# Kernel optimization log

Measured on AMD Instinct MI355X. Metric: run time of the kernel, lower is better.

The kernel has to match this reference:

```python
import jax, jax.numpy as jnp
import numpy as np

B, S, D = 2, 2048, 1024
H, KH = 16, 4            # query heads, kv heads
DK = D // H              # 64
REP = H // KH            # queries per kv head


def _rope(x):
    # x: (B, h, S, dk); non-interleaved rotate-half RoPE as in source
    dk = x.shape[-1]
    half = dk // 2
    seq = x.shape[2]
    theta = 10000.0 ** (-(jnp.arange(half, dtype=jnp.float32) / half))
    pos = jnp.arange(seq, dtype=jnp.float32)
    freqs = pos[:, None] * theta[None, :]          # (S, half)
    cos = jnp.cos(freqs)[None, None]               # (1,1,S,half)
    sin = jnp.sin(freqs)[None, None]
    x1, x2 = x[..., :half], x[..., half:]
    return jnp.concatenate([x1 * cos - x2 * sin, x2 * cos + x1 * sin], axis=-1)


def setup_inputs() -> dict:
    key = jax.random.key(0)
    ks = jax.random.split(key, 9)
    sd = 1.0 / np.sqrt(D)
    x = jax.random.normal(ks[0], (B, S, D), dtype=jnp.float32)
    # causal mask: 1 where attend allowed, 0 where masked (mask==0 -> -inf)
    mask = jnp.tril(jnp.ones((S, S), dtype=jnp.int32))[None, None]
    Wq = jax.random.normal(ks[1], (D, H * DK), dtype=jnp.float32) * sd
    bq = jnp.zeros((H * DK,), dtype=jnp.float32)
    Wk = jax.random.normal(ks[2], (D, KH * DK), dtype=jnp.float32) * sd
    bk = jnp.zeros((KH * DK,), dtype=jnp.float32)
    Wv = jax.random.normal(ks[3], (D, KH * DK), dtype=jnp.float32) * sd
    bv = jnp.zeros((KH * DK,), dtype=jnp.float32)
    Wo = jax.random.normal(ks[4], (H * DK, D), dtype=jnp.float32) * sd
    bo = jnp.zeros((D,), dtype=jnp.float32)
    return {"x": x, "mask": mask, "Wq": Wq, "bq": bq, "Wk": Wk, "bk": bk,
            "Wv": Wv, "bv": bv, "Wo": Wo, "bo": bo}


def reference(x, mask, Wq, bq, Wk, bk, Wv, bv, Wo, bo):
    b, s, _ = x.shape
    q = (x @ Wq + bq).reshape(b, s, H, DK).transpose(0, 2, 1, 3)   # (B,H,S,DK)
    k = (x @ Wk + bk).reshape(b, s, KH, DK).transpose(0, 2, 1, 3)  # (B,KH,S,DK)
    v = (x @ Wv + bv).reshape(b, s, KH, DK).transpose(0, 2, 1, 3)
    q = _rope(q)
    k = _rope(k)
    k = jnp.repeat(k, REP, axis=1)  # GQA expand: (B,H,S,DK)
    v = jnp.repeat(v, REP, axis=1)
    attn = jnp.einsum('bhqd,bhkd->bhqk', q, k) / np.sqrt(DK).astype(np.float32)
    attn = jnp.where(mask == 0, -jnp.inf, attn)
    score = jax.nn.softmax(attn, axis=-1)
    out = jnp.einsum('bhqk,bhkd->bhqd', score, v)   # (B,H,S,DK)
    out = out.transpose(0, 2, 1, 3).reshape(b, s, H * DK)
    return out @ Wo + bo
```

## Files before the change

### kernel.cpp

```cpp
#include <hip/hip_runtime.h>
#include <math.h>

#define B_   2
#define S_   2048
#define D_   1024
#define H_   16
#define KH_  4
#define DK_  64

using bf16x8 = __attribute__((ext_vector_type(8))) short;
using bf16x4 = __attribute__((ext_vector_type(4))) short;
using f32x4  = __attribute__((ext_vector_type(4))) float;
using u32x4  = __attribute__((ext_vector_type(4))) unsigned int;
using u32x2  = __attribute__((ext_vector_type(2))) unsigned int;

__device__ inline unsigned short f2bf(float f) {
    unsigned u = __float_as_uint(f);
    u += 0x7FFFu + ((u >> 16) & 1u);
    return (unsigned short)(u >> 16);
}
__device__ inline float bf2f(unsigned short u) {
    return __uint_as_float(((unsigned)u) << 16);
}

#ifdef __has_builtin
#if __has_builtin(__builtin_amdgcn_cvt_pk_bf16_f32)
#define PKBF16 1
#endif
#if __has_builtin(__builtin_amdgcn_exp2f)
#define NEXP2 1
#endif
#endif
__device__ inline unsigned pk2bf(float a, float b) {
#ifdef PKBF16
    auto r = __builtin_amdgcn_cvt_pk_bf16_f32(a, b);
    unsigned u; __builtin_memcpy(&u, &r, 4);
    return u;
#else
    return (unsigned)f2bf(a) | ((unsigned)f2bf(b) << 16);
#endif
}
__device__ inline float fexp2(float x) {
#ifdef NEXP2
    return __builtin_amdgcn_exp2f(x);
#else
    return exp2f(x);
#endif
}

#define GL16(gp, lp) __builtin_amdgcn_global_load_lds( \
    (const __attribute__((address_space(1))) unsigned int*)(gp), \
    (__attribute__((address_space(3))) unsigned int*)(lp), 16, 0, 0)

__global__ __launch_bounds__(256) void prep_kernel(
    const float* __restrict__ x,
    const float* __restrict__ Wq, const float* __restrict__ Wk,
    const float* __restrict__ Wv, const float* __restrict__ Wo,
    unsigned short* __restrict__ xb,
    unsigned short* __restrict__ WqkvT,
    unsigned short* __restrict__ WoT)
{
    __shared__ float T[64][65];
    const int t = threadIdx.x;
    int bx = blockIdx.x;

    if (bx < 2048) {
        const int i = bx * 256 + t;
        f32x4 a = *(const f32x4*)(x + (long)i * 8);
        f32x4 b = *(const f32x4*)(x + (long)i * 8 + 4);
        bf16x8 o;
        o[0] = (short)f2bf(a[0]); o[1] = (short)f2bf(a[1]);
        o[2] = (short)f2bf(a[2]); o[3] = (short)f2bf(a[3]);
        o[4] = (short)f2bf(b[0]); o[5] = (short)f2bf(b[1]);
        o[6] = (short)f2bf(b[2]); o[7] = (short)f2bf(b[3]);
        *(bf16x8*)(xb + (long)i * 8) = o;
        return;
    }
    bx -= 2048;
    const float* in; unsigned short* out; int C;
    if (bx < 256)      { in = Wq; out = WqkvT;               C = 1024; }
    else if (bx < 320) { in = Wk; out = WqkvT + 1024 * 1024; C = 256;  bx -= 256; }
    else if (bx < 384) { in = Wv; out = WqkvT + 1280 * 1024; C = 256;  bx -= 320; }
    else               { in = Wo; out = WoT;                 C = 1024; bx -= 384; }
    const int R  = 1024, nr = 16;
    const int r0 = (bx % nr) * 64;
    const int c0 = (bx / nr) * 64;
    {
        const int r  = t >> 2;
        const int cq = (t & 3) * 16;
        const float* src = in + (long)(r0 + r) * C + c0 + cq;
        #pragma unroll
        for (int i = 0; i < 4; ++i) {
            f32x4 v = *(const f32x4*)(src + i * 4);
            T[r][cq + i * 4 + 0] = v[0];
            T[r][cq + i * 4 + 1] = v[1];
            T[r][cq + i * 4 + 2] = v[2];
            T[r][cq + i * 4 + 3] = v[3];
        }
    }
    __syncthreads();
    {
        const int c  = t >> 2;
        const int rq = (t & 3) * 16;
        bf16x8 p0, p1;
        #pragma unroll
        for (int i = 0; i < 8; ++i) {
            p0[i] = (short)f2bf(T[rq + i][c]);
            p1[i] = (short)f2bf(T[rq + 8 + i][c]);
        }
        unsigned short* dst = out + (long)(c0 + c) * R + r0 + rq;
        *(bf16x8*)dst       = p0;
        *(bf16x8*)(dst + 8) = p1;
    }
}

template<bool BF16OUT>
__global__ __launch_bounds__(256) void gemm64_kernel(
    const unsigned short* __restrict__ A,
    const unsigned short* __restrict__ Bt,
    const float* __restrict__ b0,
    const float* __restrict__ b1,
    const float* __restrict__ b2,
    float* __restrict__ outf,
    unsigned short* __restrict__ outb,
    int N, int K)
{
    __shared__ unsigned short As[2][64][64];
    __shared__ unsigned short Bs[2][128][64];

    const int t  = threadIdx.x;
    const int m0 = blockIdx.x * 64;
    const int n0 = blockIdx.y * 128;

    const int w    = t >> 6;
    const int lane = t & 63;
    const int n    = lane & 15;
    const int quad = lane >> 4;
    const int wm   = (w >> 1) * 32;
    const int wn   = (w & 1) * 64;

    const int sr8 = lane >> 3;
    const int gch = (lane & 7) ^ sr8;

    const unsigned short* gA = A  + (long)(m0 + w * 8 + sr8) * K + gch * 8;
    const unsigned short* gB = Bt + (long)(n0 + w * 8 + sr8) * K + gch * 8;

    #define STAGE(buf, kk)                                              \
    do {                                                                \
        GL16(gA + (kk),              &As[buf][w * 8][0]);               \
        GL16(gA + 32 * K + (kk),     &As[buf][w * 8 + 32][0]);          \
        GL16(gB + (kk),              &Bs[buf][w * 8][0]);               \
        GL16(gB + 32 * K + (kk),     &Bs[buf][w * 8 + 32][0]);          \
        GL16(gB + 64 * K + (kk),     &Bs[buf][w * 8 + 64][0]);          \
        GL16(gB + 96 * K + (kk),     &Bs[buf][w * 8 + 96][0]);          \
    } while (0)

    STAGE(0, 0);

    f32x4 acc[2][4];
    #pragma unroll
    for (int i = 0; i < 2; ++i)
        #pragma unroll
        for (int j = 0; j < 4; ++j) acc[i][j] = 0.0f;

    const int n7 = n & 7;

    for (int k0 = 0; k0 < K; k0 += 64) {
        const int cur = (k0 >> 6) & 1;
        __syncthreads();
        if (k0 + 64 < K) STAGE(cur ^ 1, k0 + 64);

        #pragma unroll
        for (int kp = 0; kp < 2; ++kp) {
            const int ca = ((kp * 4 + quad) ^ n7) * 8;
            bf16x8 af[2], bfr[4];
            #pragma unroll
            for (int i = 0; i < 2; ++i)
                af[i] = *(const bf16x8*)&As[cur][wm + i * 16 + n][ca];
            #pragma unroll
            for (int j = 0; j < 4; ++j)
                bfr[j] = *(const bf16x8*)&Bs[cur][wn + j * 16 + n][ca];
            #pragma unroll
            for (int mi = 0; mi < 2; ++mi)
                #pragma unroll
                for (int ni = 0; ni < 4; ++ni)
                    acc[mi][ni] = __builtin_amdgcn_mfma_f32_16x16x32_bf16(
                        af[mi], bfr[ni], acc[mi][ni], 0, 0, 0);
        }
    }
    #undef STAGE

    #pragma unroll
    for (int mi = 0; mi < 2; ++mi) {
        #pragma unroll
        for (int r = 0; r < 4; ++r) {
            const int gm = m0 + wm + mi * 16 + quad * 4 + r;
            #pragma unroll
            for (int ni = 0; ni < 4; ++ni) {
                const int gn = n0 + wn + ni * 16 + n;
                if (BF16OUT) {
                    const float b = (gn < 1024) ? b0[gn]
                                  : (gn < 1280) ? b1[gn - 1024]
                                                : b2[gn - 1280];
                    outb[(long)gm * N + gn] = f2bf(acc[mi][ni][r] + b);
                } else {
                    outf[(long)gm * N + gn] = acc[mi][ni][r] + b0[gn];
                }
            }
        }
    }
}

__global__ __launch_bounds__(256) void scatter_kernel(
    const unsigned short* __restrict__ qkvm,
    unsigned short* __restrict__ qbuf,
    unsigned short* __restrict__ kbuf,
    unsigned short* __restrict__ vbuf)
{
    __shared__ unsigned short T[64][72];
    const int t = threadIdx.x;
    int bx = blockIdx.x;

    if (bx < 1280) {
        const int idx = bx * 256 + t;
        const int m   = idx / 80;
        const int rem = idx - m * 80;
        const int h20 = rem >> 2;
        const int d0  = (rem & 3) * 8;

        const int s  = m & (S_ - 1);
        const int bb = m >> 11;
        const int col0 = (h20 < 16) ? h20 * 64 + d0 : 1024 + (h20 - 16) * 64 + d0;
        const float scl = (h20 < 16) ? 0.1803368801111606f : 1.0f;

        const bf16x8 x1v = *(const bf16x8*)(qkvm + (long)m * 1536 + col0);
        const bf16x8 x2v = *(const bf16x8*)(qkvm + (long)m * 1536 + col0 + 32);
        bf16x8 o1, o2;
        #pragma unroll
        for (int j = 0; j < 8; ++j) {
            const int d = d0 + j;
            const float theta = exp2f(-(float)d * (13.287712379549449f / 32.0f));
            const float f = (float)s * theta;
            const float c = cosf(f) * scl, sn = sinf(f) * scl;
            const float x1 = bf2f((unsigned short)x1v[j]);
            const float x2 = bf2f((unsigned short)x2v[j]);
            o1[j] = (short)f2bf(x1 * c - x2 * sn);
            o2[j] = (short)f2bf(x2 * c + x1 * sn);
        }
        unsigned short* dst = (h20 < 16)
            ? qbuf + ((long)(bb * H_ + h20) * S_ + s) * DK_ + d0
            : kbuf + ((long)(bb * KH_ + (h20 - 16)) * S_ + s) * DK_ + d0;
        *(bf16x8*)dst        = o1;
        *(bf16x8*)(dst + 32) = o2;
        return;
    }
    bx -= 1280;
    const int bkh = bx >> 5;
    const int s0  = (bx & 31) * 64;
    {
        const int s  = t >> 2;
        const int dq = (t & 3) * 16;
        const unsigned short* src =
            qkvm + (long)((bkh >> 2) * S_ + s0 + s) * 1536 + 1280 + (bkh & 3) * 64 + dq;
        *(bf16x8*)&T[s][dq]     = *(const bf16x8*)src;
        *(bf16x8*)&T[s][dq + 8] = *(const bf16x8*)(src + 8);
    }
    __syncthreads();
    {
        const int d  = t >> 2;
        const int sq = (t & 3) * 16;
        bf16x8 p0, p1;
        #pragma unroll
        for (int i = 0; i < 8; ++i) {
            p0[i] = (short)T[sq + i][d];
            p1[i] = (short)T[sq + 8 + i][d];
        }
        unsigned short* dst = vbuf + ((long)bkh * DK_ + d) * S_ + s0 + sq;
        *(bf16x8*)dst       = p0;
        *(bf16x8*)(dst + 8) = p1;
    }
}

__global__ __launch_bounds__(512) void attn_kernel(
    const unsigned short* __restrict__ qb,
    const unsigned short* __restrict__ kbf,
    const unsigned short* __restrict__ vT,
    unsigned short* __restrict__ ot)
{
    __shared__ __align__(16) unsigned short Ks[2][64][64];
    __shared__ __align__(16) unsigned short Vs[2][64][64];
    __shared__ __align__(16) unsigned short Ps[8][16][64];

    const int tid = threadIdx.x;
    const int bx  = blockIdx.x;

    const int j  = bx >> 8;
    const int p  = bx & 255;
    const int g  = p >> 5;
    const int bh = p & 31;
    const int a  = j ? g : (15 - g);

    const int b   = bh >> 4, h = bh & 15;
    const int kh  = h >> 2;
    const int q0  = a * 128;

    const int wv   = tid >> 6;
    const int lane = tid & 63;
    const int n    = lane & 15;
    const int quad = lane >> 4;
    const int xk   = n & 7;

    const unsigned short* qp =
        qb + ((long)(b * H_ + h) * S_ + q0 + wv * 16 + n) * DK_;
    const bf16x8 qa0 = *(const bf16x8*)(qp + quad * 8);
    const bf16x8 qa1 = *(const bf16x8*)(qp + 32 + quad * 8);

    f32x4 O[4];
    #pragma unroll
    for (int dt = 0; dt < 4; ++dt) O[dt] = 0.0f;
    float lsum = 0.f;

    const unsigned short* kbase = kbf + (long)(b * KH_ + kh) * S_ * DK_;
    const unsigned short* vbase = vT  + (long)(b * KH_ + kh) * DK_ * S_;

    const int ntiles = 2 * a + 2;
    const int ub     = 2 * a + (wv >> 2);
    const int srow = tid >> 3;
    const int lc   = tid & 7;
    const int sc8  = lc * 8;
    const int pcs  = (lc ^ (srow & 7)) * 8;

    u32x4 kr = *(const u32x4*)(kbase + (long)srow * DK_ + sc8);
    u32x4 vr = *(const u32x4*)(vbase + (long)srow * S_ + sc8);
    *(u32x4*)&Ks[0][srow][pcs] = kr;
    *(u32x4*)&Vs[0][srow][pcs] = vr;

    for (int u = 0; u < ntiles; ++u) {
        const int cur = u & 1;
        const int kb  = u * 64;
        __syncthreads();

        if (u + 1 < ntiles) {
            const int kbn = kb + 64;
            kr = *(const u32x4*)(kbase + (long)(kbn + srow) * DK_ + sc8);
            vr = *(const u32x4*)(vbase + (long)srow * S_ + kbn + sc8);
        }

        if (u <= ub) {
            f32x4 sc[4];
            #pragma unroll
            for (int ct = 0; ct < 4; ++ct) {
                const bf16x8 kf0 =
                    *(const bf16x8*)&Ks[cur][ct * 16 + n][(quad ^ xk) * 8];
                const bf16x8 kf1 =
                    *(const bf16x8*)&Ks[cur][ct * 16 + n][((quad + 4) ^ xk) * 8];
                f32x4 c = 0.0f;
                c = __builtin_amdgcn_mfma_f32_16x16x32_bf16(kf0, qa0, c, 0, 0, 0);
                c = __builtin_amdgcn_mfma_f32_16x16x32_bf16(kf1, qa1, c, 0, 0, 0);
                sc[ct] = c;
            }

            if (u == ub) {
                const int qg = q0 + wv * 16 + n;
                #pragma unroll
                for (int ct = 0; ct < 4; ++ct) {
                    const int kq = kb + ct * 16 + quad * 4;
                    #pragma unroll
                    for (int r = 0; r < 4; ++r)
                        if (kq + r > qg) sc[ct][r] = -INFINITY;
                }
            }

            f32x4 rs4 = 0.0f;
            #pragma unroll
            for (int ct = 0; ct < 4; ++ct) {
                #pragma unroll
                for (int r = 0; r < 4; ++r) {
                    const float p2 = fexp2(sc[ct][r]);
                    sc[ct][r] = p2;
                    rs4[r] += p2;
                }
            }
            lsum += (rs4[0] + rs4[1]) + (rs4[2] + rs4[3]);

            #pragma unroll
            for (int ct = 0; ct < 4; ++ct) {
                u32x2 pw;
                pw[0] = pk2bf(sc[ct][0], sc[ct][1]);
                pw[1] = pk2bf(sc[ct][2], sc[ct][3]);
                const int pc = ((2 * ct + (quad >> 1)) ^ xk) * 8 + (quad & 1) * 4;
                *(u32x2*)&Ps[wv][n][pc] = pw;
            }
            const bf16x8 pb0 = *(const bf16x8*)&Ps[wv][n][(quad ^ xk) * 8];
            const bf16x8 pb1 = *(const bf16x8*)&Ps[wv][n][((quad + 4) ^ xk) * 8];

            #pragma unroll
            for (int dt = 0; dt < 4; ++dt) {
                const bf16x8 av0 =
                    *(const bf16x8*)&Vs[cur][dt * 16 + n][(quad ^ xk) * 8];
                const bf16x8 av1 =
                    *(const bf16x8*)&Vs[cur][dt * 16 + n][((quad + 4) ^ xk) * 8];
                O[dt] = __builtin_amdgcn_mfma_f32_16x16x32_bf16(av0, pb0, O[dt], 0, 0, 0);
                O[dt] = __builtin_amdgcn_mfma_f32_16x16x32_bf16(av1, pb1, O[dt], 0, 0, 0);
            }
        }

        if (u + 1 < ntiles) {
            const int nb = cur ^ 1;
            *(u32x4*)&Ks[nb][srow][pcs] = kr;
            *(u32x4*)&Vs[nb][srow][pcs] = vr;
        }
    }

    lsum += __shfl_xor(lsum, 16);
    lsum += __shfl_xor(lsum, 32);
    const float inv = 1.0f / lsum;
    #pragma unroll
    for (int dt = 0; dt < 4; ++dt) {
        u32x2 pw;
        pw[0] = pk2bf(O[dt][0] * inv, O[dt][1] * inv);
        pw[1] = pk2bf(O[dt][2] * inv, O[dt][3] * inv);
        const int pc = ((2 * dt + (quad >> 1)) ^ xk) * 8 + (quad & 1) * 4;
        *(u32x2*)&Ps[wv][n][pc] = pw;
    }
    __builtin_amdgcn_s_waitcnt(0);
    const int fr = lane >> 3;
    const int c8l = lane & 7;
    #pragma unroll
    for (int it = 0; it < 2; ++it) {
        const int row = it * 8 + fr;
        const int q   = q0 + wv * 16 + row;
        unsigned short* op = ot + ((long)(b * S_ + q) * H_ + h) * DK_ + c8l * 8;
        *(bf16x8*)op = *(const bf16x8*)&Ps[wv][row][(c8l ^ fr) * 8];
    }
}

extern "C" void kernel_launch(void* const* d_in, const int* in_sizes, int n_in,
                              void* d_out, int out_size, void* d_ws, size_t ws_size,
                              hipStream_t stream)
{
    const float* x  = (const float*)d_in[0];
    const float* Wq = (const float*)d_in[2];
    const float* bq = (const float*)d_in[3];
    const float* Wk = (const float*)d_in[4];
    const float* bk = (const float*)d_in[5];
    const float* Wv = (const float*)d_in[6];
    const float* bv = (const float*)d_in[7];
    const float* Wo = (const float*)d_in[8];
    const float* bo = (const float*)d_in[9];
    float* out = (float*)d_out;

    unsigned short* ws    = (unsigned short*)d_ws;
    unsigned short* xb    = ws;
    unsigned short* qkvm  = xb + 4194304;
    unsigned short* qbuf  = qkvm + 6291456;
    unsigned short* kbuf  = qbuf + 4194304;
    unsigned short* vbuf  = kbuf + 1048576;
    unsigned short* WqkvT = vbuf + 1048576;
    unsigned short* WoT   = WqkvT + 1572864;
    unsigned short* ob    = qkvm;

    prep_kernel<<<2688, 256, 0, stream>>>(x, Wq, Wk, Wv, Wo, xb, WqkvT, WoT);

    gemm64_kernel<true><<<dim3(64, 12), 256, 0, stream>>>(
        xb, WqkvT, bq, bk, bv, nullptr, qkvm, 1536, 1024);

    scatter_kernel<<<1536, 256, 0, stream>>>(qkvm, qbuf, kbuf, vbuf);

    attn_kernel<<<512, 512, 0, stream>>>(qbuf, kbuf, vbuf, ob);

    gemm64_kernel<false><<<dim3(64, 8), 256, 0, stream>>>(
        ob, WoT, bo, nullptr, nullptr, out, nullptr, 1024, 1024);
}
```

Before: 177.2 us.

## Fuse RoPE and Q/K head scatter into QKV GEMM epilogue with cos/sin table

Moves the RoPE rotation and the Q/K head-major scatter out of the separate scatter kernel and into the QKV projection GEMM epilogue. Each wave's 64-column tile is exactly one head, so the rotate-half pairs are in registers. A cos/sin table is precomputed in extra prep_kernel blocks, so the epilogue no longer calls transcendentals. The scatter kernel now only transposes V, which removes one full read and write of Q/K through the qkvm buffer. In exchange, the epilogue stores are scalar 2-byte writes spread across head-major rows, which may coalesce poorly, and the table adds extra global loads.

```diff
diff --git a/kernel.cpp b/kernel.cpp
--- a/kernel.cpp
+++ b/kernel.cpp
@@ -11,6 +11,7 @@
 using bf16x8 = __attribute__((ext_vector_type(8))) short;
 using bf16x4 = __attribute__((ext_vector_type(4))) short;
 using f32x4  = __attribute__((ext_vector_type(4))) float;
+using f32x2  = __attribute__((ext_vector_type(2))) float;
 using u32x4  = __attribute__((ext_vector_type(4))) unsigned int;
 using u32x2  = __attribute__((ext_vector_type(2))) unsigned int;
 
@@ -58,7 +59,8 @@
     const float* __restrict__ Wv, const float* __restrict__ Wo,
     unsigned short* __restrict__ xb,
     unsigned short* __restrict__ WqkvT,
-    unsigned short* __restrict__ WoT)
+    unsigned short* __restrict__ WoT,
+    float* __restrict__ sct)
 {
     __shared__ float T[64][65];
     const int t = threadIdx.x;
@@ -74,6 +76,15 @@
         o[4] = (short)f2bf(b[0]); o[5] = (short)f2bf(b[1]);
         o[6] = (short)f2bf(b[2]); o[7] = (short)f2bf(b[3]);
         *(bf16x8*)(xb + (long)i * 8) = o;
+        return;
+    }
+    if (bx >= 2688) {
+        const int idx = (bx - 2688) * 256 + t;
+        const int s = idx >> 5, d = idx & 31;
+        const float theta = exp2f(-(float)d * (13.287712379549449f / 32.0f));
+        const float f = (float)s * theta;
+        sct[(long)idx * 2]     = cosf(f);
+        sct[(long)idx * 2 + 1] = sinf(f);
         return;
     }
     bx -= 2048;
@@ -123,6 +134,9 @@
     const float* __restrict__ b2,
     float* __restrict__ outf,
     unsigned short* __restrict__ outb,
+    unsigned short* __restrict__ qbuf,
+    unsigned short* __restrict__ kbuf,
+    const float* __restrict__ sct,
     int N, int K)
 {
     __shared__ unsigned short As[2][64][64];
@@ -190,20 +204,65 @@
     }
     #undef STAGE
 
-    #pragma unroll
-    for (int mi = 0; mi < 2; ++mi) {
-        #pragma unroll
-        for (int r = 0; r < 4; ++r) {
-            const int gm = m0 + wm + mi * 16 + quad * 4 + r;
-            #pragma unroll
-            for (int ni = 0; ni < 4; ++ni) {
-                const int gn = n0 + wn + ni * 16 + n;
-                if (BF16OUT) {
-                    const float b = (gn < 1024) ? b0[gn]
-                                  : (gn < 1280) ? b1[gn - 1024]
-                                                : b2[gn - 1280];
-                    outb[(long)gm * N + gn] = f2bf(acc[mi][ni][r] + b);
-                } else {
+    if (BF16OUT) {
+        const int colbase = n0 + wn;
+        if (colbase < 1280) {
+            const bool isQ = colbase < 1024;
+            const float scl = isQ ? 0.1803368801111606f : 1.0f;
+            const int hh = isQ ? (colbase >> 6) : ((colbase - 1024) >> 6);
+            const int HH = isQ ? H_ : KH_;
+            unsigned short* obase = isQ ? qbuf : kbuf;
+            const int gn0 = colbase + n;
+            const float bA = isQ ? b0[gn0]      : b1[gn0 - 1024];
+            const float bB = isQ ? b0[gn0 + 16] : b1[gn0 - 1008];
+            const float bC = isQ ? b0[gn0 + 32] : b1[gn0 - 992];
+            const float bD = isQ ? b0[gn0 + 48] : b1[gn0 - 976];
+            #pragma unroll
+            for (int mi = 0; mi < 2; ++mi) {
+                #pragma unroll
+                for (int r = 0; r < 4; ++r) {
+                    const int gm = m0 + wm + mi * 16 + quad * 4 + r;
+                    const int bb = gm >> 11, s = gm & (S_ - 1);
+                    const f32x2 t0 = *(const f32x2*)(sct + ((long)s * 32 + n) * 2);
+                    const f32x2 t1 = *(const f32x2*)(sct + ((long)s * 32 + 16 + n) * 2);
+                    const float c0 = t0[0] * scl, s0v = t0[1] * scl;
+                    const float c1 = t1[0] * scl, s1v = t1[1] * scl;
+                    const float x1 = acc[mi][0][r] + bA;
+                    const float y1 = acc[mi][1][r] + bB;
+                    const float x2 = acc[mi][2][r] + bC;
+                    const float y2 = acc[mi][3][r] + bD;
+                    unsigned short* dst =
+                        obase + ((long)(bb * HH + hh) * S_ + s) * DK_;
+                    dst[n]      = f2bf(x1 * c0 - x2 * s0v);
+                    dst[16 + n] = f2bf(y1 * c1 - y2 * s1v);
+                    dst[32 + n] = f2bf(x2 * c0 + x1 * s0v);
+                    dst[48 + n] = f2bf(y2 * c1 + y1 * s1v);
+                }
+            }
+        } else {
+            #pragma unroll
+            for (int mi = 0; mi < 2; ++mi) {
+                #pragma unroll
+                for (int r = 0; r < 4; ++r) {
+                    const int gm = m0 + wm + mi * 16 + quad * 4 + r;
+                    #pragma unroll
+                    for (int ni = 0; ni < 4; ++ni) {
+                        const int gn = colbase + ni * 16 + n;
+                        outb[(long)gm * N + gn] =
+                            f2bf(acc[mi][ni][r] + b2[gn - 1280]);
+                    }
+                }
+            }
+        }
+    } else {
+        #pragma unroll
+        for (int mi = 0; mi < 2; ++mi) {
+            #pragma unroll
+            for (int r = 0; r < 4; ++r) {
+                const int gm = m0 + wm + mi * 16 + quad * 4 + r;
+                #pragma unroll
+                for (int ni = 0; ni < 4; ++ni) {
+                    const int gn = n0 + wn + ni * 16 + n;
                     outf[(long)gm * N + gn] = acc[mi][ni][r] + b0[gn];
                 }
             }
@@ -213,48 +272,11 @@
 
 __global__ __launch_bounds__(256) void scatter_kernel(
     const unsigned short* __restrict__ qkvm,
-    unsigned short* __restrict__ qbuf,
-    unsigned short* __restrict__ kbuf,
     unsigned short* __restrict__ vbuf)
 {
     __shared__ unsigned short T[64][72];
     const int t = threadIdx.x;
-    int bx = blockIdx.x;
-
-    if (bx < 1280) {
-        const int idx = bx * 256 + t;
-        const int m   = idx / 80;
-        const int rem = idx - m * 80;
-        const int h20 = rem >> 2;
-        const int d0  = (rem & 3) * 8;
-
-        const int s  = m & (S_ - 1);
-        const int bb = m >> 11;
-        const int col0 = (h20 < 16) ? h20 * 64 + d0 : 1024 + (h20 - 16) * 64 + d0;
-        const float scl = (h20 < 16) ? 0.1803368801111606f : 1.0f;
-
-        const bf16x8 x1v = *(const bf16x8*)(qkvm + (long)m * 1536 + col0);
-        const bf16x8 x2v = *(const bf16x8*)(qkvm + (long)m * 1536 + col0 + 32);
-        bf16x8 o1, o2;
-        #pragma unroll
-        for (int j = 0; j < 8; ++j) {
-            const int d = d0 + j;
-            const float theta = exp2f(-(float)d * (13.287712379549449f / 32.0f));
-            const float f = (float)s * theta;
-            const float c = cosf(f) * scl, sn = sinf(f) * scl;
-            const float x1 = bf2f((unsigned short)x1v[j]);
-            const float x2 = bf2f((unsigned short)x2v[j]);
-            o1[j] = (short)f2bf(x1 * c - x2 * sn);
-            o2[j] = (short)f2bf(x2 * c + x1 * sn);
-        }
-        unsigned short* dst = (h20 < 16)
-            ? qbuf + ((long)(bb * H_ + h20) * S_ + s) * DK_ + d0
-            : kbuf + ((long)(bb * KH_ + (h20 - 16)) * S_ + s) * DK_ + d0;
-        *(bf16x8*)dst        = o1;
-        *(bf16x8*)(dst + 32) = o2;
-        return;
-    }
-    bx -= 1280;
+    const int bx = blockIdx.x;
     const int bkh = bx >> 5;
     const int s0  = (bx & 31) * 64;
     {
@@ -458,17 +480,19 @@
     unsigned short* vbuf  = kbuf + 1048576;
     unsigned short* WqkvT = vbuf + 1048576;
     unsigned short* WoT   = WqkvT + 1572864;
+    float*          sct   = (float*)(WoT + 1048576);
     unsigned short* ob    = qkvm;
 
-    prep_kernel<<<2688, 256, 0, stream>>>(x, Wq, Wk, Wv, Wo, xb, WqkvT, WoT);
+    prep_kernel<<<2944, 256, 0, stream>>>(x, Wq, Wk, Wv, Wo, xb, WqkvT, WoT, sct);
 
     gemm64_kernel<true><<<dim3(64, 12), 256, 0, stream>>>(
-        xb, WqkvT, bq, bk, bv, nullptr, qkvm, 1536, 1024);
-
-    scatter_kernel<<<1536, 256, 0, stream>>>(qkvm, qbuf, kbuf, vbuf);
+        xb, WqkvT, bq, bk, bv, nullptr, qkvm, qbuf, kbuf, sct, 1536, 1024);
+
+    scatter_kernel<<<256, 256, 0, stream>>>(qkvm, vbuf);
 
     attn_kernel<<<512, 512, 0, stream>>>(qbuf, kbuf, vbuf, ob);
 
     gemm64_kernel<false><<<dim3(64, 8), 256, 0, stream>>>(
-        ob, WoT, bo, nullptr, nullptr, out, nullptr, 1024, 1024);
-}
+        ob, WoT, bo, nullptr, nullptr, out, nullptr, nullptr, nullptr, nullptr,
+        1024, 1024);
+}
```

After: 168.1 us. 5.1% less time.
